# Performance work log

Measured on AMD Instinct MI355X. Metric: run time of the kernel, lower is better.

Reference implementation:

```python
import jax, jax.numpy as jnp
import numpy as np

EPS = 1.1920929e-07  # torch F.rms_norm default eps for fp32
D, NH, NKV, HD = 1024, 16, 4, 64
MLP_MULT, L = 3, 6           # L = num_layers // 2 shared blocks
VS, HS, LS, ROPE_B = 50257, 4096, 30.0, 10000.0
B, S = 2, 2048


def rmsn(x):
    return x * jax.lax.rsqrt(jnp.mean(jnp.square(x), -1, keepdims=True) + EPS)


def rope_tables(s):
    f = 1.0 / ROPE_B ** (jnp.arange(0, HD, 2, dtype=jnp.float32) / HD)
    fr = jnp.outer(jnp.arange(s, dtype=jnp.float32), f)  # [s, HD/2]
    return jnp.cos(fr), jnp.sin(fr)


def rot(x, c, s):
    h = x.shape[-1] // 2
    x1, x2 = x[..., :h], x[..., h:]
    return jnp.concatenate([x1 * c + x2 * s, -x1 * s + x2 * c], -1)


def attn(x, Wq, Wk, Wv, Wo, qg, cos, sin):
    b, s, d = x.shape
    q = (x @ Wq.T).reshape(b, s, NH, HD).swapaxes(1, 2)    # [b,nh,s,hd]
    k = (x @ Wk.T).reshape(b, s, NKV, HD).swapaxes(1, 2)   # [b,nkv,s,hd]
    v = (x @ Wv.T).reshape(b, s, NKV, HD).swapaxes(1, 2)
    q, k = rmsn(q), rmsn(k)                                # QK RMSNorm (no weight)
    c, si = cos[None, None], sin[None, None]
    q, k = rot(q, c, si), rot(k, c, si)
    q = q * qg[None, :, None, None]                        # per-head gate
    g = NH // NKV
    qr = q.reshape(b, NKV, g, s, HD)
    scores = jnp.einsum('bkgqd,bksd->bkgqs', qr, k) / jnp.sqrt(jnp.float32(HD))
    mask = jnp.tril(jnp.ones((s, s), bool))
    scores = jnp.where(mask, scores, -jnp.inf)
    p = jax.nn.softmax(scores, -1)
    y = jnp.einsum('bkgqs,bksd->bkgqd', p, v).reshape(b, NH, s, HD)
    y = y.swapaxes(1, 2).reshape(b, s, d)
    return y @ Wo.T


def mlp(x, Wf, Wo2):
    return jnp.square(jax.nn.relu(x @ Wf.T)) @ Wo2.T       # ReLU^2 MLP


def block(x, x0, p, cos, sin):
    Wq, Wk, Wv, Wo, qg, a_sc, m_sc, rm, Wf, Wo2 = p
    x = rm[0] * x + rm[1] * x0                             # learned residual mix
    x = x + a_sc * attn(rmsn(x), Wq, Wk, Wv, Wo, qg, cos, sin)
    x = x + m_sc * mlp(rmsn(x), Wf, Wo2)
    return x


def setup_inputs() -> dict:
    key = jax.random.key(0)
    ks = jax.random.split(key, 16)
    sd = 0.02
    return {
        'ids': jax.random.randint(ks[0], (B, S), 0, VS, dtype=jnp.int32),
        'y': jax.random.randint(ks[1], (B, S), 0, VS, dtype=jnp.int32),
        'u_emb': jax.random.normal(ks[2], (VS, D // 2), jnp.float32) * 0.02,
        'b_emb': jax.random.normal(ks[3], (HS, D // 2), jnp.float32) * 0.01,
        'Wq': jax.random.normal(ks[4], (L, D, D), jnp.float32) * sd,
        'Wk': jax.random.normal(ks[5], (L, NKV * HD, D), jnp.float32) * sd,
        'Wv': jax.random.normal(ks[6], (L, NKV * HD, D), jnp.float32) * sd,
        'Wo': jax.random.normal(ks[7], (L, D, D), jnp.float32) * sd,
        'qg': jnp.ones((L, NH), jnp.float32),
        'a_scale': jnp.ones((L, D), jnp.float32),
        'm_scale': jnp.ones((L, D), jnp.float32),
        'rm': jnp.stack([jnp.full((L, D), 0.7, jnp.float32), jnp.full((L, D), 0.3, jnp.float32)], 1),
        'Wf': jax.random.normal(ks[8], (L, MLP_MULT * D, D), jnp.float32) * sd,
        'Wo2': jax.random.normal(ks[9], (L, D, MLP_MULT * D), jnp.float32) * sd,
        'sw': jnp.ones((L, D), jnp.float32),
    }


def reference(ids, y, u_emb, b_emb, Wq, Wk, Wv, Wo, qg, a_scale, m_scale, rm, Wf, Wo2, sw):
    b, s = ids.shape
    # BigramHash embedding: (prev_id*VS + id) % HS, computed mod-HS to stay in int32
    pi = jnp.pad(ids[:, :-1], ((0, 0), (1, 0)))
    bi = (((pi % HS) * (VS % HS)) % HS + ids % HS) % HS
    h = jnp.concatenate([u_emb[ids], b_emb[bi]], -1)       # [b,s,D]
    h = rmsn(h)
    cos, sin = rope_tables(s)
    h0, sk = h, []
    for i in range(L):                                     # encoder half
        p = (Wq[i], Wk[i], Wv[i], Wo[i], qg[i], a_scale[i], m_scale[i], rm[i], Wf[i], Wo2[i])
        h = block(h, h0, p, cos, sin)
        sk.append(h)
    for i in range(L):                                     # decoder half (reversed blocks, skips)
        h = h + sw[i] * sk[L - 1 - i]
        j = L - 1 - i
        p = (Wq[j], Wk[j], Wv[j], Wo[j], qg[j], a_scale[j], m_scale[j], rm[j], Wf[j], Wo2[j])
        h = block(h, h0, p, cos, sin)
    h = rmsn(h)
    # tied bigram-hash head: out_weight = [u_emb | zeros]  ->  only first D/2 dims matter
    lg = h.reshape(-1, D)[:, :D // 2] @ u_emb.T            # [b*s, VS]
    lg = LS * jnp.tanh(lg / LS)                            # logit softcap
    logp = jax.nn.log_softmax(lg.astype(jnp.float32), -1)
    yf = y.reshape(-1)
    loss = -jnp.mean(jnp.take_along_axis(logp, yf[:, None], 1)[:, 0])
    return loss
```

## Files before the change

### kernel.cpp

```cpp
#include <hip/hip_runtime.h>
#include <cstdint>
#include <cstddef>

constexpr int   Dm    = 1024;
constexpr int   NHn   = 16;
constexpr int   NKVn  = 4;
constexpr int   HDn   = 64;
constexpr int   Ln    = 6;
constexpr int   Sn    = 2048;
constexpr int   Bn    = 2;
constexpr int   ROWS  = Bn * Sn;
constexpr int   VSn   = 50257;
constexpr int   HSn   = 4096;
constexpr float EPSF  = 1.1920929e-07f;
constexpr int   VCHUNK = 4096;
constexpr int   VPAD   = 50304;
constexpr float LOG2E  = 1.44269504f;

#define DEV __device__ __forceinline__

typedef __attribute__((ext_vector_type(8))) short bf16x8;
typedef __attribute__((ext_vector_type(4))) float f32x4;
using ush = unsigned short;

DEV ush f2bf(float f) {
    unsigned int u = __float_as_uint(f);
    u = (u + 0x7fffu + ((u >> 16) & 1u)) >> 16;
    return (ush)u;
}

DEV float b2f(ush v) {
    return __uint_as_float(((unsigned int)v) << 16);
}

DEV f32x4 mfma16(bf16x8 a, bf16x8 b, f32x4 c) {
    return __builtin_amdgcn_mfma_f32_16x16x32_bf16(a, b, c, 0, 0, 0);
}

DEV void llds16(const ush* g, ush* l) {
    __builtin_amdgcn_global_load_lds(
        (const __attribute__((address_space(1))) void*)g,
        (__attribute__((address_space(3))) void*)l, 16, 0, 0);
}

DEV float block_sum256(float v, float* red) {
#pragma unroll
    for (int off = 32; off; off >>= 1) v += __shfl_xor(v, off);
    __syncthreads();
    if ((threadIdx.x & 63) == 0) red[threadIdx.x >> 6] = v;
    __syncthreads();
    return red[0] + red[1] + red[2] + red[3];
}

DEV float block_max256(float v, float* red) {
#pragma unroll
    for (int off = 32; off; off >>= 1) v = fmaxf(v, __shfl_xor(v, off));
    __syncthreads();
    if ((threadIdx.x & 63) == 0) red[threadIdx.x >> 6] = v;
    __syncthreads();
    return fmaxf(fmaxf(red[0], red[1]), fmaxf(red[2], red[3]));
}

__global__ void rope_kernel(float* __restrict__ cb, float* __restrict__ sb) {
    int idx = blockIdx.x * 256 + threadIdx.x;
    if (idx >= Sn * 32) return;
    int t = idx >> 5, f = idx & 31;
    float freq = powf(10000.f, -(float)f * (1.f / 32.f));
    float ang  = (float)t * freq;
    cb[idx] = cosf(ang);
    sb[idx] = sinf(ang);
}

__global__ void cvt_bf16_kernel(const float* __restrict__ s, ush* __restrict__ d, int n4) {
    int i = blockIdx.x * 256 + threadIdx.x;
    if (i >= n4) return;
    float4 v = *(const float4*)(s + (size_t)i * 4);
    ushort4 o;
    o.x = f2bf(v.x); o.y = f2bf(v.y); o.z = f2bf(v.z); o.w = f2bf(v.w);
    *(ushort4*)(d + (size_t)i * 4) = o;
}

__global__ void zpad_kernel(ush* __restrict__ p, int n) {
    int i = blockIdx.x * 256 + threadIdx.x;
    if (i < n) p[i] = 0;
}

__global__ __launch_bounds__(256)
void embed_kernel(const int* __restrict__ ids, const float* __restrict__ ue,
                  const float* __restrict__ be, float* __restrict__ h,
                  float* __restrict__ h0) {
    __shared__ float red[4];
    int r = blockIdx.x;
    int s = r % Sn;
    int id = ids[r];
    int prev = (s == 0) ? 0 : ids[r - 1];
    int bi = ((prev % HSn) * (VSn % HSn) % HSn + id % HSn) % HSn;
    int tid = threadIdx.x;
    float vals[4];
    float ss = 0.f;
#pragma unroll
    for (int t = 0; t < 4; ++t) {
        int j = tid + t * 256;
        float v = (j < 512) ? ue[(size_t)id * 512 + j]
                            : be[(size_t)bi * 512 + (j - 512)];
        vals[t] = v; ss += v * v;
    }
    ss = block_sum256(ss, red);
    float rinv = rsqrtf(ss * (1.f / Dm) + EPSF);
#pragma unroll
    for (int t = 0; t < 4; ++t) {
        int j = tid + t * 256;
        float v = vals[t] * rinv;
        h [(size_t)r * Dm + j] = v;
        h0[(size_t)r * Dm + j] = v;
    }
}

template<bool SKIP>
__global__ __launch_bounds__(256)
void resmix_kernel(float* __restrict__ h, const float* __restrict__ h0,
                   const float* __restrict__ rm0, ush* __restrict__ xnb,
                   const ush* __restrict__ skb, const float* __restrict__ sw) {
    __shared__ float red[4];
    int r = blockIdx.x, tid = threadIdx.x;
    const float* rm1 = rm0 + Dm;
    float vals[4]; float ss = 0.f;
#pragma unroll
    for (int t = 0; t < 4; ++t) {
        int j = tid + t * 256;
        size_t o = (size_t)r * Dm + j;
        float base = h[o];
        if (SKIP) base = fmaf(sw[j], b2f(skb[o]), base);
        float v = rm0[j] * base + rm1[j] * h0[o];
        vals[t] = v; ss += v * v;
        h[o] = v;
    }
    ss = block_sum256(ss, red);
    float rinv = rsqrtf(ss * (1.f / Dm) + EPSF);
#pragma unroll
    for (int t = 0; t < 4; ++t)
        xnb[(size_t)r * Dm + tid + t * 256] = f2bf(vals[t] * rinv);
}

__global__ __launch_bounds__(256)
void rmsn_kernel(const float* __restrict__ x, ush* __restrict__ out) {
    __shared__ float red[4];
    int r = blockIdx.x, tid = threadIdx.x;
    float vals[4]; float ss = 0.f;
#pragma unroll
    for (int t = 0; t < 4; ++t) {
        float v = x[(size_t)r * Dm + tid + t * 256];
        vals[t] = v; ss += v * v;
    }
    ss = block_sum256(ss, red);
    float rinv = rsqrtf(ss * (1.f / Dm) + EPSF);
#pragma unroll
    for (int t = 0; t < 4; ++t)
        out[(size_t)r * Dm + tid + t * 256] = f2bf(vals[t] * rinv);
}

template<int TM, int MODE>
__global__ __launch_bounds__(256)
void gemm_k(const ush* __restrict__ A, const ush* __restrict__ B,
            ush* __restrict__ C, int M, int N, int K,
            int lda, int ldb, int ldc,
            float* __restrict__ hres, const float* __restrict__ sc,
            ush* __restrict__ dup) {
    __shared__ __align__(16) ush As[TM * 32];
    __shared__ __align__(16) ush Bs[128 * 32];
    const int m0 = blockIdx.x * TM, n0 = blockIdx.y * 128;
    const int tid  = threadIdx.x;
    const int w    = tid >> 6, lane = tid & 63;
    const int l15  = lane & 15, quad = lane >> 4;
    const int wr   = w >> 1, wc = w & 1;
    constexpr int NI = TM / 32;

    const int srow = lane >> 2, sch = lane & 3;
    const ush* Ag;
    ush* AsW;
    if constexpr (TM == 128) {
        Ag  = A + (size_t)(m0 + w * 32 + srow) * lda + sch * 8;
        AsW = As + w * 1024;
    } else {
        Ag  = A + (size_t)(m0 + w * 16 + srow) * lda + sch * 8;
        AsW = As + w * 512;
    }
    const ush* Bg = B + (size_t)(n0 + w * 32 + srow) * ldb + sch * 8;
    ush* BsW = Bs + w * 1024;

    f32x4 acc[NI][4] = {};

    for (int k0 = 0; k0 < K; k0 += 32) {
        __syncthreads();
        llds16(Ag + k0, AsW);
        if constexpr (TM == 128) llds16(Ag + k0 + 16 * lda, AsW + 512);
        llds16(Bg + k0,            BsW);
        llds16(Bg + k0 + 16 * ldb, BsW + 512);
        __syncthreads();
        bf16x8 af[NI], bfv[4];
#pragma unroll
        for (int i = 0; i < NI; ++i)
            af[i] = *(const bf16x8*)&As[(wr * (TM / 2) + i * 16 + l15) * 32 + quad * 8];
#pragma unroll
        for (int j = 0; j < 4; ++j)
            bfv[j] = *(const bf16x8*)&Bs[(wc * 64 + j * 16 + l15) * 32 + quad * 8];
#pragma unroll
        for (int i = 0; i < NI; ++i)
#pragma unroll
            for (int j = 0; j < 4; ++j)
                acc[i][j] = mfma16(af[i], bfv[j], acc[i][j]);
    }

#pragma unroll
    for (int i = 0; i < NI; ++i) {
#pragma unroll
        for (int j = 0; j < 4; ++j) {
            int row = m0 + wr * (TM / 2) + i * 16 + quad * 4;
            int col = n0 + wc * 64 + j * 16 + l15;
#pragma unroll
            for (int r = 0; r < 4; ++r) {
                float v = acc[i][j][r];
                if (MODE == 1) { v = fmaxf(v, 0.f); v = v * v; }
                else if (MODE == 2) {
                    float ax = fabsf(v) * (1.f / 30.f);
                    float e  = __expf(-2.f * ax);
                    float t  = (1.f - e) / (1.f + e);
                    v = copysignf(t * 30.f, v);
                }
                if (MODE == 3) {
                    size_t o = (size_t)(row + r) * ldc + col;
                    float nv = fmaf(sc[col], v, hres[o]);
                    hres[o] = nv;
                    if (dup) dup[o] = f2bf(nv);
                } else {
                    C[(size_t)(row + r) * ldc + col] = f2bf(v);
                }
            }
        }
    }
}

__global__ __launch_bounds__(256)
void qknorm_rope_kernel(const ush* __restrict__ in,
                        ush* __restrict__ qout, ush* __restrict__ kout,
                        const float* __restrict__ cosb, const float* __restrict__ sinb,
                        const float* __restrict__ qg) {
    int idx  = blockIdx.x * 4 + (threadIdx.x >> 6);
    int lane = threadIdx.x & 63;
    int t, hh, in_off;
    ush* outp; int out_ld;
    bool isq = idx < ROWS * NHn;
    if (isq) { t = idx >> 4; hh = idx & 15; in_off = hh * 64; outp = qout; out_ld = 1024; }
    else { int i2 = idx - ROWS * NHn; t = i2 >> 2; hh = i2 & 3; in_off = 1024 + hh * 64; outp = kout; out_ld = 256; }
    int sidx = t % Sn;
    float x = b2f(in[(size_t)t * 1536 + in_off + lane]);
    float ss = x * x;
#pragma unroll
    for (int off = 32; off; off >>= 1) ss += __shfl_xor(ss, off);
    float xn = x * rsqrtf(ss * (1.f / HDn) + EPSF);
    float partner = __shfl_xor(xn, 32);
    int f = lane & 31;
    float c  = cosb[sidx * 32 + f];
    float sv = sinb[sidx * 32 + f];
    float o = (lane < 32) ? fmaf(xn, c, partner * sv)
                          : fmaf(xn, c, -partner * sv);
    if (isq) o *= qg[hh] * (0.125f * LOG2E);
    outp[(size_t)t * out_ld + hh * 64 + lane] = f2bf(o);
}

__global__ __launch_bounds__(256)
void vtrans_kernel(const ush* __restrict__ in, ush* __restrict__ out) {
    __shared__ ush tile[32][33];
    int s0 = blockIdx.x * 32;
    int c0 = blockIdx.y * 32;
    int i = threadIdx.x >> 5;
    int j = threadIdx.x & 31;
#pragma unroll
    for (int k = 0; k < 4; ++k)
        tile[i + k * 8][j] = in[(size_t)(s0 + i + k * 8) * 1536 + 1280 + c0 + j];
    __syncthreads();
#pragma unroll
    for (int k = 0; k < 4; ++k)
        out[(size_t)(c0 + i + k * 8) * (size_t)ROWS + s0 + j] = tile[j][i + k * 8];
}

__global__ __launch_bounds__(256)
void attn_mfma_kernel(const ush* __restrict__ qb,
                      const ush* __restrict__ kb,
                      const ush* __restrict__ vt,
                      ush* __restrict__ opart,
                      float* __restrict__ lpart,
                      const float* __restrict__ qgl) {
    __shared__ __align__(16) ush Ks[64 * 72];
    __shared__ __align__(16) ush Vs[64 * 72];
    __shared__ __align__(16) unsigned int PsD[128 * 36];
    const int pair = blockIdx.x % 40;
    const int bh   = blockIdx.x / 40;
    const int h    = bh & 15;
    const int b    = bh >> 4;
    const int g    = (pair >= 24) ? 3 : (pair >= 12) ? 2 : (pair >= 4) ? 1 : 0;
    const int off_p = pair - 2 * g * (g + 1);
    const int t    = 4 * g + off_p / (g + 1);
    const int c    = off_p % (g + 1);
    const int kvh  = h >> 2;
    const int w    = threadIdx.x >> 6, lane = threadIdx.x & 63;
    const int l15  = lane & 15, quad = lane >> 4;
    const int q0   = t * 128;
    const int k_lo = c * 512;
    const int k_hi_full = (t + 1) * 128;
    const int k_hi = (k_lo + 512 < k_hi_full) ? (k_lo + 512) : k_hi_full;
    const int nblk = (k_hi - k_lo) >> 6;
    const float mfix = 8.f * fabsf(qgl[h]) * LOG2E;

    bf16x8 qf[2][2];
    {
        size_t qr = (size_t)(b * Sn + q0 + w * 32 + l15) * 1024 + h * 64;
        qf[0][0] = *(const bf16x8*)(qb + qr + quad * 8);
        qf[0][1] = *(const bf16x8*)(qb + qr + 32 + quad * 8);
        qf[1][0] = *(const bf16x8*)(qb + qr + 16 * 1024 + quad * 8);
        qf[1][1] = *(const bf16x8*)(qb + qr + 16 * 1024 + 32 + quad * 8);
    }
    f32x4 Oacc[2][4] = {};
    float lsum[2][4] = {{0.f,0.f,0.f,0.f},{0.f,0.f,0.f,0.f}};

    const int rrS = threadIdx.x >> 3, chS = threadIdx.x & 7;
    const size_t kbase = (size_t)(b * Sn) * 256 + kvh * 64;
    const size_t vbase = (size_t)(kvh * 64) * (size_t)ROWS + b * Sn;

    uint4 kr0 = *(const uint4*)(kb + kbase + (size_t)(k_lo + rrS) * 256 + chS * 8);
    uint4 kr1 = *(const uint4*)(kb + kbase + (size_t)(k_lo + rrS + 32) * 256 + chS * 8);
    uint4 vr0 = *(const uint4*)(vt + vbase + (size_t)rrS * ROWS + k_lo + chS * 8);
    uint4 vr1 = *(const uint4*)(vt + vbase + (size_t)(rrS + 32) * ROWS + k_lo + chS * 8);

    for (int kb_i = 0; kb_i < nblk; ++kb_i) {
        const int k0 = k_lo + kb_i * 64;
        __syncthreads();
        *(uint4*)&Ks[rrS * 72 + chS * 8]        = kr0;
        *(uint4*)&Ks[(rrS + 32) * 72 + chS * 8] = kr1;
        *(uint4*)&Vs[rrS * 72 + chS * 8]        = vr0;
        *(uint4*)&Vs[(rrS + 32) * 72 + chS * 8] = vr1;
        __syncthreads();
        if (kb_i + 1 < nblk) {
            int k0n = k0 + 64;
            kr0 = *(const uint4*)(kb + kbase + (size_t)(k0n + rrS) * 256 + chS * 8);
            kr1 = *(const uint4*)(kb + kbase + (size_t)(k0n + rrS + 32) * 256 + chS * 8);
            vr0 = *(const uint4*)(vt + vbase + (size_t)rrS * ROWS + k0n + chS * 8);
            vr1 = *(const uint4*)(vt + vbase + (size_t)(rrS + 32) * ROWS + k0n + chS * 8);
        }

        f32x4 S0[4] = {}, S1[4] = {};
#pragma unroll
        for (int cc = 0; cc < 4; ++cc) {
            bf16x8 kf0 = *(const bf16x8*)&Ks[(cc * 16 + l15) * 72 + quad * 8];
            bf16x8 kf1 = *(const bf16x8*)&Ks[(cc * 16 + l15) * 72 + 32 + quad * 8];
            S0[cc] = mfma16(qf[0][0], kf0, S0[cc]);
            S0[cc] = mfma16(qf[0][1], kf1, S0[cc]);
            S1[cc] = mfma16(qf[1][0], kf0, S1[cc]);
            S1[cc] = mfma16(qf[1][1], kf1, S1[cc]);
        }

#pragma unroll
        for (int f = 0; f < 2; ++f) {
            f32x4* S = f ? S1 : S0;
            const int qbF = q0 + w * 32 + f * 16;
            if (k0 + 63 > qbF) {
#pragma unroll
                for (int cc = 0; cc < 4; ++cc) {
                    int key = k0 + cc * 16 + l15;
#pragma unroll
                    for (int r = 0; r < 4; ++r)
                        if (key > qbF + quad * 4 + r) S[cc][r] = -INFINITY;
                }
            }
#pragma unroll
            for (int cc = 0; cc < 4; ++cc)
#pragma unroll
                for (int r = 0; r < 4; ++r) {
                    float p = exp2f(S[cc][r] - mfix);
                    S[cc][r] = p;
                    lsum[f][r] += p;
                }
            const int prow = w * 32 + f * 16 + quad * 4;
#pragma unroll
            for (int cp = 0; cp < 2; ++cp)
#pragma unroll
                for (int r = 0; r < 4; ++r) {
                    unsigned int pk = __builtin_amdgcn_perm(
                        __float_as_uint(S[cp + 2][r]), __float_as_uint(S[cp][r]),
                        0x07060302u);
                    PsD[(prow + r) * 36 + cp * 16 + l15] = pk;
                }
        }

#pragma unroll
        for (int f = 0; f < 2; ++f) {
            const int prow = w * 32 + f * 16 + l15;
            unsigned int d[8];
            *(uint4*)&d[0] = *(const uint4*)&PsD[prow * 36 + quad * 8];
            *(uint4*)&d[4] = *(const uint4*)&PsD[prow * 36 + quad * 8 + 4];
            unsigned int lo[4], hi[4];
#pragma unroll
            for (int tt = 0; tt < 4; ++tt) {
                lo[tt] = __builtin_amdgcn_perm(d[2 * tt + 1], d[2 * tt], 0x05040100u);
                hi[tt] = __builtin_amdgcn_perm(d[2 * tt + 1], d[2 * tt], 0x07060302u);
            }
            bf16x8 pf0 = *(const bf16x8*)lo;
            bf16x8 pf1 = *(const bf16x8*)hi;
#pragma unroll
            for (int dt = 0; dt < 4; ++dt) {
                bf16x8 vf0 = *(const bf16x8*)&Vs[(dt * 16 + l15) * 72 + quad * 8];
                bf16x8 vf1 = *(const bf16x8*)&Vs[(dt * 16 + l15) * 72 + 32 + quad * 8];
                Oacc[f][dt] = mfma16(pf0, vf0, Oacc[f][dt]);
                Oacc[f][dt] = mfma16(pf1, vf1, Oacc[f][dt]);
            }
        }
    }

#pragma unroll
    for (int f = 0; f < 2; ++f) {
#pragma unroll
        for (int m = 1; m <= 8; m <<= 1)
#pragma unroll
            for (int r = 0; r < 4; ++r)
                lsum[f][r] += __shfl_xor(lsum[f][r], m);
#pragma unroll
        for (int r = 0; r < 4; ++r) {
            int token = b * Sn + q0 + w * 32 + f * 16 + quad * 4 + r;
            if (l15 == 0)
                lpart[((size_t)c * ROWS + token) * NHn + h] = lsum[f][r];
#pragma unroll
            for (int dt = 0; dt < 4; ++dt)
                opart[((size_t)c * ROWS + token) * 1024 + h * 64 + dt * 16 + l15]
                    = f2bf(Oacc[f][dt][r]);
        }
    }
}

__global__ __launch_bounds__(256)
void attn_combine_kernel(const ush* __restrict__ opart,
                         const float* __restrict__ lpart,
                         ush* __restrict__ attb) {
    int token = blockIdx.x;
    int j = threadIdx.x * 4;
    int head = j >> 6;
    int nc = ((token % Sn) >> 9) + 1;
    float a0 = 0.f, a1 = 0.f, a2 = 0.f, a3 = 0.f, l = 0.f;
    for (int cc = 0; cc < nc; ++cc) {
        ushort4 o4 = *(const ushort4*)(opart + ((size_t)cc * ROWS + token) * 1024 + j);
        a0 += b2f(o4.x); a1 += b2f(o4.y); a2 += b2f(o4.z); a3 += b2f(o4.w);
        l  += lpart[((size_t)cc * ROWS + token) * NHn + head];
    }
    float rin = 1.f / l;
    ushort4 out;
    out.x = f2bf(a0 * rin); out.y = f2bf(a1 * rin);
    out.z = f2bf(a2 * rin); out.w = f2bf(a3 * rin);
    *(ushort4*)(attb + (size_t)token * 1024 + j) = out;
}

__global__ void loss_init_kernel(float* __restrict__ m, float* __restrict__ s,
                                 float* __restrict__ tg) {
    int i = blockIdx.x * 256 + threadIdx.x;
    if (i < ROWS) { m[i] = -INFINITY; s[i] = 0.f; tg[i] = 0.f; }
}

__global__ __launch_bounds__(256)
void chunk_reduce_kernel(const ush* __restrict__ Cc, int Nc, int c0,
                         const int* __restrict__ y, float* __restrict__ m,
                         float* __restrict__ s, float* __restrict__ tg) {
    __shared__ float red[4];
    int r = blockIdx.x, tid = threadIdx.x;
    const ush* row = Cc + (size_t)r * VCHUNK;
    float v[16];
    float mx = -INFINITY;
#pragma unroll
    for (int t = 0; t < 16; ++t) {
        int j = tid + t * 256;
        v[t] = (j < Nc) ? b2f(row[j]) : -INFINITY;
        mx = fmaxf(mx, v[t]);
    }
    mx = block_max256(mx, red);
    float se = 0.f;
#pragma unroll
    for (int t = 0; t < 16; ++t)
        se += __expf(v[t] - mx);
    se = block_sum256(se, red);
    if (tid == 0) {
        float mo = m[r];
        float mn = fmaxf(mo, mx);
        s[r] = s[r] * __expf(mo - mn) + se * __expf(mx - mn);
        m[r] = mn;
        int t = y[r] - c0;
        if (t >= 0 && t < Nc) tg[r] = b2f(row[t]);
    }
}

__global__ __launch_bounds__(256)
void loss_final_kernel(const float* __restrict__ m, const float* __restrict__ s,
                       const float* __restrict__ tg, float* __restrict__ out) {
    __shared__ float red[4];
    float part = 0.f;
    for (int r = threadIdx.x; r < ROWS; r += 256)
        part += m[r] + logf(s[r]) - tg[r];
    part = block_sum256(part, red);
    if (threadIdx.x == 0) out[0] = part * (1.f / ROWS);
}

extern "C" void kernel_launch(void* const* d_in, const int* in_sizes, int n_in,
                              void* d_out, int out_size, void* d_ws, size_t ws_size,
                              hipStream_t stream) {
    const int*   ids = (const int*)d_in[0];
    const int*   yv  = (const int*)d_in[1];
    const float* ue  = (const float*)d_in[2];
    const float* be  = (const float*)d_in[3];
    const float* Wq  = (const float*)d_in[4];
    const float* Wk  = (const float*)d_in[5];
    const float* Wv  = (const float*)d_in[6];
    const float* Wo  = (const float*)d_in[7];
    const float* qg  = (const float*)d_in[8];
    const float* asc = (const float*)d_in[9];
    const float* msc = (const float*)d_in[10];
    const float* rm  = (const float*)d_in[11];
    const float* Wf  = (const float*)d_in[12];
    const float* Wo2 = (const float*)d_in[13];
    const float* sw  = (const float*)d_in[14];
    (void)in_sizes; (void)n_in; (void)out_size; (void)ws_size;

    char* wsb = (char*)d_ws;
    size_t off = 0;
    auto alloc = [&](size_t bytes) {
        void* p = (void*)(wsb + off);
        off += ((bytes + 255) & ~size_t(255));
        return p;
    };
    float* h    = (float*)alloc((size_t)ROWS * Dm * 4);
    float* h0   = (float*)alloc((size_t)ROWS * Dm * 4);
    float* cosb = (float*)alloc((size_t)Sn * 32 * 4);
    float* sinb = (float*)alloc((size_t)Sn * 32 * 4);
    float* mrow = (float*)alloc(ROWS * 4);
    float* srow = (float*)alloc(ROWS * 4);
    float* tgv  = (float*)alloc(ROWS * 4);
    float* lpart= (float*)alloc((size_t)4 * ROWS * NHn * 4);
    ush* skb  = (ush*)alloc((size_t)Ln * ROWS * Dm * 2);
    ush* xnb  = (ush*)alloc((size_t)ROWS * Dm * 2);
    ush* qkvb = (ush*)alloc((size_t)ROWS * 1536 * 2);
    ush* hidb = (ush*)alloc((size_t)ROWS * 3 * Dm * 2);
    ush* opart = qkvb;
    ush* qbf  = (ush*)alloc((size_t)ROWS * Dm * 2);
    ush* kbf  = (ush*)alloc((size_t)ROWS * 256 * 2);
    ush* vtb  = (ush*)alloc((size_t)256 * ROWS * 2);
    ush* attb = (ush*)alloc((size_t)ROWS * Dm * 2);
    ush* wall = (ush*)alloc((size_t)Ln * 8704 * 1024 * 2);
    ush* ueb  = (ush*)alloc((size_t)VPAD * 512 * 2);
    ush* chunk = skb;

    auto cvt = [&](const float* s, ush* d, size_t n) {
        int n4 = (int)(n / 4);
        cvt_bf16_kernel<<<(n4 + 255) / 256, 256, 0, stream>>>(s, d, n4);
    };

    for (int l = 0; l < Ln; ++l) {
        ush* wl = wall + (size_t)l * 8704 * 1024;
        cvt(Wq + (size_t)l * Dm * Dm,      wl,              (size_t)Dm * Dm);
        cvt(Wk + (size_t)l * 256 * Dm,     wl + 1024 * Dm,  (size_t)256 * Dm);
        cvt(Wv + (size_t)l * 256 * Dm,     wl + 1280 * Dm,  (size_t)256 * Dm);
        cvt(Wo + (size_t)l * Dm * Dm,      wl + 1536 * Dm,  (size_t)Dm * Dm);
        cvt(Wf + (size_t)l * 3 * Dm * Dm,  wl + 2560 * Dm,  (size_t)3 * Dm * Dm);
        cvt(Wo2 + (size_t)l * 3 * Dm * Dm, wl + 5632 * Dm,  (size_t)3 * Dm * Dm);
    }
    cvt(ue, ueb, (size_t)VSn * 512);
    zpad_kernel<<<((VPAD - VSn) * 512 + 255) / 256, 256, 0, stream>>>(
        ueb + (size_t)VSn * 512, (VPAD - VSn) * 512);

    rope_kernel<<<(Sn * 32 + 255) / 256, 256, 0, stream>>>(cosb, sinb);
    embed_kernel<<<ROWS, 256, 0, stream>>>(ids, ue, be, h, h0);

    auto run_block = [&](int l, ush* dup, const ush* skip, const float* swv) {
        ush* wl    = wall + (size_t)l * 8704 * 1024;
        ush* wqkvb = wl;
        ush* wob   = wl + (size_t)1536 * 1024;
        ush* wfb   = wl + (size_t)2560 * 1024;
        ush* wo2b  = wl + (size_t)5632 * 1024;

        if (skip)
            resmix_kernel<true><<<ROWS, 256, 0, stream>>>(
                h, h0, rm + (size_t)l * 2 * Dm, xnb, skip, swv);
        else
            resmix_kernel<false><<<ROWS, 256, 0, stream>>>(
                h, h0, rm + (size_t)l * 2 * Dm, xnb, nullptr, nullptr);
        gemm_k<64, 0><<<dim3(ROWS / 64, 1536 / 128), 256, 0, stream>>>(
            xnb, wqkvb, qkvb, ROWS, 1536, Dm, Dm, Dm, 1536, nullptr, nullptr, nullptr);
        qknorm_rope_kernel<<<ROWS * (NHn + NKVn) / 4, 256, 0, stream>>>(
            qkvb, qbf, kbf, cosb, sinb, qg + (size_t)l * NHn);
        vtrans_kernel<<<dim3(ROWS / 32, 8), 256, 0, stream>>>(qkvb, vtb);
        attn_mfma_kernel<<<Bn * NHn * 40, 256, 0, stream>>>(
            qbf, kbf, vtb, opart, lpart, qg + (size_t)l * NHn);
        attn_combine_kernel<<<ROWS, 256, 0, stream>>>(opart, lpart, attb);
        gemm_k<64, 3><<<dim3(ROWS / 64, Dm / 128), 256, 0, stream>>>(
            attb, wob, nullptr, ROWS, Dm, Dm, Dm, Dm, Dm,
            h, asc + (size_t)l * Dm, nullptr);
        rmsn_kernel<<<ROWS, 256, 0, stream>>>(h, xnb);
        gemm_k<128, 1><<<dim3(ROWS / 128, 3 * Dm / 128), 256, 0, stream>>>(
            xnb, wfb, hidb, ROWS, 3 * Dm, Dm, Dm, Dm, 3 * Dm, nullptr, nullptr, nullptr);
        gemm_k<64, 3><<<dim3(ROWS / 64, Dm / 128), 256, 0, stream>>>(
            hidb, wo2b, nullptr, ROWS, Dm, 3 * Dm, 3 * Dm, 3 * Dm, Dm,
            h, msc + (size_t)l * Dm, dup);
    };

    for (int l = 0; l < Ln; ++l)
        run_block(l, skb + (size_t)l * ROWS * Dm, nullptr, nullptr);
    for (int i = 0; i < Ln; ++i) {
        int j = Ln - 1 - i;
        run_block(j, nullptr, skb + (size_t)j * ROWS * Dm, sw + (size_t)i * Dm);
    }

    rmsn_kernel<<<ROWS, 256, 0, stream>>>(h, xnb);
    loss_init_kernel<<<(ROWS + 255) / 256, 256, 0, stream>>>(mrow, srow, tgv);
    for (int c0 = 0; c0 < VSn; c0 += VCHUNK) {
        int Nc = (VSn - c0 < VCHUNK) ? (VSn - c0) : VCHUNK;
        int Ng = (VPAD - c0 < VCHUNK) ? (VPAD - c0) : VCHUNK;
        gemm_k<128, 2><<<dim3(ROWS / 128, Ng / 128), 256, 0, stream>>>(
            xnb, ueb + (size_t)c0 * 512, chunk, ROWS, Ng, 512, Dm, 512, VCHUNK,
            nullptr, nullptr, nullptr);
        chunk_reduce_kernel<<<ROWS, 256, 0, stream>>>(chunk, Nc, c0, yv, mrow, srow, tgv);
    }
    loss_final_kernel<<<1, 256, 0, stream>>>(mrow, srow, tgv, (float*)d_out);
}
```

Baseline: 4.192 ms.

## Triple-buffer GEMM LDS tiles with async prefetch and XOR-swizzled layout

The bf16 MFMA GEMM kernel now keeps three LDS buffers and issues global-to-LDS loads two k-steps ahead. It waits with explicit vmcnt counts and a single barrier per iteration instead of two __syncthreads around each synchronous load. The loads and fragment reads also use an XOR swizzle on the 16-byte chunk index to reduce LDS bank conflicts. This hides global load latency behind MFMA work, but triples the LDS footprint, which may lower occupancy, and relies on hand-counted waitcnt values being correct.

Result: faster. 4.078 ms (-2.7%).

```diff
diff --git a/kernel.cpp b/kernel.cpp
--- a/kernel.cpp
+++ b/kernel.cpp
@@ -43,6 +43,12 @@
         (__attribute__((address_space(3))) void*)l, 16, 0, 0);
 }
 
+DEV void bar() {
+    asm volatile("" ::: "memory");
+    __builtin_amdgcn_s_barrier();
+    asm volatile("" ::: "memory");
+}
+
 DEV float block_sum256(float v, float* red) {
 #pragma unroll
     for (int off = 32; off; off >>= 1) v += __shfl_xor(v, off);
@@ -166,8 +172,9 @@
             int lda, int ldb, int ldc,
             float* __restrict__ hres, const float* __restrict__ sc,
             ush* __restrict__ dup) {
-    __shared__ __align__(16) ush As[TM * 32];
-    __shared__ __align__(16) ush Bs[128 * 32];
+    constexpr int ASZ = TM * 32;
+    __shared__ __align__(16) ush As[3][ASZ];
+    __shared__ __align__(16) ush Bs[3][128 * 32];
     const int m0 = blockIdx.x * TM, n0 = blockIdx.y * 128;
     const int tid  = threadIdx.x;
     const int w    = tid >> 6, lane = tid & 63;
@@ -175,40 +182,67 @@
     const int wr   = w >> 1, wc = w & 1;
     constexpr int NI = TM / 32;
 
-    const int srow = lane >> 2, sch = lane & 3;
+    const int srow = lane >> 2;
+    const int schs = (lane & 3) ^ ((srow >> 1) & 3);
     const ush* Ag;
-    ush* AsW;
+    int aoff;
     if constexpr (TM == 128) {
-        Ag  = A + (size_t)(m0 + w * 32 + srow) * lda + sch * 8;
-        AsW = As + w * 1024;
+        Ag   = A + (size_t)(m0 + w * 32 + srow) * lda + schs * 8;
+        aoff = w * 1024;
     } else {
-        Ag  = A + (size_t)(m0 + w * 16 + srow) * lda + sch * 8;
-        AsW = As + w * 512;
-    }
-    const ush* Bg = B + (size_t)(n0 + w * 32 + srow) * ldb + sch * 8;
-    ush* BsW = Bs + w * 1024;
+        Ag   = A + (size_t)(m0 + w * 16 + srow) * lda + schs * 8;
+        aoff = w * 512;
+    }
+    const ush* Bg  = B + (size_t)(n0 + w * 32 + srow) * ldb + schs * 8;
+    const int boff = w * 1024;
+
+    auto stage = [&](int buf, int k0) {
+        llds16(Ag + k0, &As[buf][aoff]);
+        if constexpr (TM == 128) llds16(Ag + k0 + 16 * lda, &As[buf][aoff + 512]);
+        llds16(Bg + k0,            &Bs[buf][boff]);
+        llds16(Bg + k0 + 16 * ldb, &Bs[buf][boff + 512]);
+    };
 
     f32x4 acc[NI][4] = {};
-
-    for (int k0 = 0; k0 < K; k0 += 32) {
-        __syncthreads();
-        llds16(Ag + k0, AsW);
-        if constexpr (TM == 128) llds16(Ag + k0 + 16 * lda, AsW + 512);
-        llds16(Bg + k0,            BsW);
-        llds16(Bg + k0 + 16 * ldb, BsW + 512);
-        __syncthreads();
+    const int nt = K >> 5;
+
+    stage(0, 0);
+    if (nt > 1) {
+        stage(1, 32);
+        if constexpr (TM == 128) asm volatile("s_waitcnt vmcnt(4)" ::: "memory");
+        else                     asm volatile("s_waitcnt vmcnt(3)" ::: "memory");
+    } else {
+        asm volatile("s_waitcnt vmcnt(0)" ::: "memory");
+    }
+    bar();
+
+    const int cso = (quad ^ ((l15 >> 1) & 3)) * 8;
+    int bcur = 0;
+    for (int t = 0; t < nt; ++t) {
+        if (t + 2 < nt) {
+            int bn = bcur >= 1 ? bcur - 1 : 2;
+            stage(bn, (t + 2) * 32);
+        }
         bf16x8 af[NI], bfv[4];
 #pragma unroll
         for (int i = 0; i < NI; ++i)
-            af[i] = *(const bf16x8*)&As[(wr * (TM / 2) + i * 16 + l15) * 32 + quad * 8];
+            af[i] = *(const bf16x8*)&As[bcur][(wr * (TM / 2) + i * 16 + l15) * 32 + cso];
 #pragma unroll
         for (int j = 0; j < 4; ++j)
-            bfv[j] = *(const bf16x8*)&Bs[(wc * 64 + j * 16 + l15) * 32 + quad * 8];
+            bfv[j] = *(const bf16x8*)&Bs[bcur][(wc * 64 + j * 16 + l15) * 32 + cso];
 #pragma unroll
         for (int i = 0; i < NI; ++i)
 #pragma unroll
             for (int j = 0; j < 4; ++j)
                 acc[i][j] = mfma16(af[i], bfv[j], acc[i][j]);
+        if (t + 2 < nt) {
+            if constexpr (TM == 128) asm volatile("s_waitcnt vmcnt(4)" ::: "memory");
+            else                     asm volatile("s_waitcnt vmcnt(3)" ::: "memory");
+        } else {
+            asm volatile("s_waitcnt vmcnt(0)" ::: "memory");
+        }
+        bar();
+        bcur = bcur == 2 ? 0 : bcur + 1;
     }
 
 #pragma unroll
```
